# Optimization experiments

Measured on AMD Instinct MI355X. Metric: run time of the kernel, lower is better.

## Reference

```python
import jax, jax.numpy as jnp
import numpy as np

MAXV = 8  # convex quad clipped by 4 half-planes has <= 8 vertices


def decode(enc, anchors):
    """ResidualCoder.decode_torch for 7-dof lidar boxes (x,y,z,dx,dy,dz,r)."""
    xa, ya, za, dxa, dya, dza, ra = [anchors[..., i] for i in range(7)]
    xt, yt, zt, dxt, dyt, dzt, rt = [enc[..., i] for i in range(7)]
    diag = jnp.sqrt(dxa * dxa + dya * dya)
    xg = xt * diag + xa
    yg = yt * diag + ya
    zg = zt * dza + za
    dxg = jnp.exp(dxt) * dxa
    dyg = jnp.exp(dyt) * dya
    dzg = jnp.exp(dzt) * dza
    rg = rt + ra
    return jnp.stack([xg, yg, zg, dxg, dyg, dzg, rg], axis=-1)


def bev_corners(boxes):
    # boxes (...,7) -> CCW BEV corners (...,4,2) using x,y,dx,dy,heading
    x, y, dx, dy, r = boxes[..., 0], boxes[..., 1], boxes[..., 3], boxes[..., 4], boxes[..., 6]
    cx = jnp.stack([dx, -dx, -dx, dx], -1) * 0.5
    cy = jnp.stack([dy, dy, -dy, -dy], -1) * 0.5
    c, s = jnp.cos(r)[..., None], jnp.sin(r)[..., None]
    px = cx * c - cy * s + x[..., None]
    py = cx * s + cy * c + y[..., None]
    return jnp.stack([px, py], -1)


def _clip(poly, n, A, B):
    """Sutherland-Hodgman clip of polygon (poly[:n]) by half-plane left of A->B."""
    idx = jnp.arange(MAXV)
    e = B - A
    s = e[0] * (poly[:, 1] - A[1]) - e[1] * (poly[:, 0] - A[0])  # signed side
    prev = (idx - 1) % jnp.maximum(n, 1)
    s_prev = s[prev]
    p_prev = poly[prev]
    active = idx < n
    cin = s >= 0
    pin = s_prev >= 0
    den = s_prev - s
    t = s_prev / jnp.where(den == 0, 1.0, den)
    inter = p_prev + t[:, None] * (poly - p_prev)
    f_int = active & (cin != pin)   # edge crosses boundary -> emit intersection
    f_cur = active & cin            # current vertex inside -> emit it
    cand = jnp.stack([inter, poly], 1).reshape(2 * MAXV, 2)
    flags = jnp.stack([f_int, f_cur], 1).reshape(2 * MAXV)
    pos = jnp.cumsum(flags) - 1
    new_n = pos[-1] + 1
    pos = jnp.where(flags, pos, MAXV)  # invalid -> dump slot
    out = jnp.zeros((MAXV + 1, 2), poly.dtype).at[pos].set(cand)[:MAXV]
    return out, new_n.astype(jnp.int32)


def _pair_iou_bev(c1, c2, a1, a2):
    # c1,c2: (4,2) CCW corners of the two rotated BEV boxes; a1,a2: scalar areas
    poly = jnp.zeros((MAXV, 2), c1.dtype).at[:4].set(c1)
    n = jnp.asarray(4, jnp.int32)
    for e in range(4):
        poly, n = _clip(poly, n, c2[e], c2[(e + 1) % 4])
    idx = jnp.arange(MAXV)
    nxt = (idx + 1) % jnp.maximum(n, 1)
    x, y = poly[:, 0], poly[:, 1]
    contrib = jnp.where(idx < n, x * y[nxt] - x[nxt] * y, 0.0)
    inter = 0.5 * jnp.abs(contrib.sum())
    return inter / jnp.clip(a1 + a2 - inter, 1e-6, None)


def rotated_iou_bev_diag(boxes1, boxes2):
    """Diagonal (elementwise) rotated BEV IoU for flattened (M,7) lidar boxes."""
    c1 = bev_corners(boxes1)
    c2 = bev_corners(boxes2)
    a1 = boxes1[..., 3] * boxes1[..., 4]
    a2 = boxes2[..., 3] * boxes2[..., 4]
    return jax.vmap(_pair_iou_bev)(c1, c2, a1, a2)


def setup_inputs() -> dict:
    key = jax.random.key(0)
    ks = jax.random.split(key, 8)
    B, N = 4, 262144
    iou_preds = jax.random.normal(ks[0], (B, N), jnp.float32)
    one_hot_targets = jax.random.randint(ks[1], (B, N), 0, 2, jnp.int32)
    weights = jax.random.uniform(ks[2], (B, N), jnp.float32)
    # realistic anchors: xy in [-50,50], z ~ -1, dims in [1.5,4.5], heading in [0,pi)
    xy = jax.random.uniform(ks[3], (N, 2), jnp.float32, -50.0, 50.0)
    z = jnp.full((N, 1), -1.0, jnp.float32)
    dims = jax.random.uniform(ks[4], (N, 3), jnp.float32, 1.5, 4.5)
    ang = jax.random.uniform(ks[5], (N, 1), jnp.float32, 0.0, np.pi)
    anchors = jnp.concatenate([xy, z, dims, ang], axis=-1)
    box_preds = 0.1 * jax.random.normal(ks[6], (B, N, 7), jnp.float32)
    reg_targets = 0.1 * jax.random.normal(ks[7], (B, N, 7), jnp.float32)
    return {"iou_preds": iou_preds, "one_hot_targets": one_hot_targets,
            "weights": weights, "anchors": anchors,
            "box_preds": box_preds, "reg_targets": reg_targets}


def reference(iou_preds, one_hot_targets, weights, anchors, box_preds, reg_targets):
    B, N = iou_preds.shape
    dec_pred = decode(box_preds, anchors[None, :, :])   # (B,N,7)
    dec_tgt = decode(reg_targets, anchors[None, :, :])  # (B,N,7)
    iou = rotated_iou_bev_diag(dec_pred.reshape(B * N, 7),
                               dec_tgt.reshape(B * N, 7)).reshape(B, N)
    # label is computed with no grad, only at positive anchors; zero elsewhere
    target = jax.lax.stop_gradient(jnp.where(one_hot_targets > 0, iou, 0.0))
    # faithful to the original quirk: BCE-with-logits applied to sigmoid(iou_preds)
    z = jax.nn.sigmoid(iou_preds)
    p_t = jnp.logaddexp(0.0, z) - z * target  # log(1+e^z) - t*z
    return p_t * weights
```

## Files before the change

kernel.cpp:

```cpp
#include <hip/hip_runtime.h>
#include <math.h>

#define BLK 256


__device__ __forceinline__ float clamp_mag(float x) {
    return copysignf(fmaxf(fabsf(x), 1e-30f), x);
}

__device__ __forceinline__ void edge_piece(float px, float py, float ex, float ey,
                                           float rx, float ry, float hx, float hy,
                                           float& area2, float& Dx, float& Dy)
{
    float sx0 = (-hx - px) * rx, sx1 = (hx - px) * rx;
    float sy0 = (-hy - py) * ry, sy1 = (hy - py) * ry;
    float smin = fmaxf(fmaxf(fminf(sx0, sx1), fminf(sy0, sy1)), 0.0f);
    float smax = fminf(fminf(fmaxf(sx0, sx1), fmaxf(sy0, sy1)), 1.0f);
    smax = fmaxf(smax, smin);
    float ax = fmaf(smin, ex, px), ay = fmaf(smin, ey, py);
    float bx = fmaf(smax, ex, px), by = fmaf(smax, ey, py);
    float ux = bx - ax, uy = by - ay;
    area2 += fmaf(ax, uy, -(ay * ux));
    Dx += ux; Dy += uy;
}

__device__ __forceinline__ float pair_loss(const float bp[5], const float rt[5],
                                           float xa, float ya, float dxa, float dya,
                                           float ra, float diag,
                                           float ip, int oh, float w)
{
    float x1  = fmaf(bp[0], diag, xa);
    float y1  = fmaf(bp[1], diag, ya);
    float dx1 = __expf(bp[2]) * dxa;
    float dy1 = __expf(bp[3]) * dya;
    float r1  = bp[4] + ra;

    float x2  = fmaf(rt[0], diag, xa);
    float y2  = fmaf(rt[1], diag, ya);
    float dx2 = __expf(rt[2]) * dxa;
    float dy2 = __expf(rt[3]) * dya;
    float r2  = rt[4] + ra;

    float a1 = dx1 * dy1, a2 = dx2 * dy2;
    float h1x = 0.5f * dx1, h1y = 0.5f * dy1;
    float h2x = 0.5f * dx2, h2y = 0.5f * dy2;

    float c2v = __cosf(r2), s2v = __sinf(r2);
    float dr  = r1 - r2;
    float cd  = __cosf(dr), sd = __sinf(dr);
    float ddx = x1 - x2, ddy = y1 - y2;
    float tx  = fmaf(c2v, ddx,  s2v * ddy);
    float ty  = fmaf(-s2v, ddx, c2v * ddy);

    float ux_ = h1x * cd,  uy_ = h1x * sd;
    float vx_ = -h1y * sd, vy_ = h1y * cd;
    float eux = 2.0f * ux_, euy = 2.0f * uy_;
    float evx = 2.0f * vx_, evy = 2.0f * vy_;
    float ruxP = __fdividef(1.0f, clamp_mag(eux));
    float ruyP = __fdividef(1.0f, clamp_mag(euy));
    float rvxP = __fdividef(1.0f, clamp_mag(evx));
    float rvyP = __fdividef(1.0f, clamp_mag(evy));
    float p0x = tx + ux_ + vx_, p0y = ty + uy_ + vy_;
    float p1x = tx - ux_ + vx_, p1y = ty - uy_ + vy_;
    float p2x = tx - ux_ - vx_, p2y = ty - uy_ - vy_;
    float p3x = tx + ux_ - vx_, p3y = ty + uy_ - vy_;

    float area2 = 0.0f, dDx = 0.0f, dDy = 0.0f;
    edge_piece(p0x, p0y, -eux, -euy, -ruxP, -ruyP, h2x, h2y, area2, dDx, dDy);
    edge_piece(p1x, p1y, -evx, -evy, -rvxP, -rvyP, h2x, h2y, area2, dDx, dDy);
    edge_piece(p2x, p2y,  eux,  euy,  ruxP,  ruyP, h2x, h2y, area2, dDx, dDy);
    edge_piece(p3x, p3y,  evx,  evy,  rvxP,  rvyP, h2x, h2y, area2, dDx, dDy);

    float upx = h2x * cd,  upy = -h2x * sd;
    float vpx = h2y * sd,  vpy = h2y * cd;
    float ox  = -(fmaf(cd, tx,  sd * ty));
    float oy  = -(fmaf(-sd, tx, cd * ty));
    float equx = 2.0f * upx, equy = 2.0f * upy;
    float eqvx = 2.0f * vpx, eqvy = 2.0f * vpy;
    float ruxQ = __fdividef(1.0f, clamp_mag(equx));
    float ruyQ = __fdividef(1.0f, clamp_mag(equy));
    float rvxQ = __fdividef(1.0f, clamp_mag(eqvx));
    float rvyQ = __fdividef(1.0f, clamp_mag(eqvy));
    float q0x = ox + upx + vpx, q0y = oy + upy + vpy;
    float q1x = ox - upx + vpx, q1y = oy - upy + vpy;
    float q2x = ox - upx - vpx, q2y = oy - upy - vpy;
    float q3x = ox + upx - vpx, q3y = oy + upy - vpy;

    float Dx = 0.0f, Dy = 0.0f;
    edge_piece(q0x, q0y, -equx, -equy, -ruxQ, -ruyQ, h1x, h1y, area2, Dx, Dy);
    edge_piece(q1x, q1y, -eqvx, -eqvy, -rvxQ, -rvyQ, h1x, h1y, area2, Dx, Dy);
    edge_piece(q2x, q2y,  equx,  equy,  ruxQ,  ruyQ, h1x, h1y, area2, Dx, Dy);
    edge_piece(q3x, q3y,  eqvx,  eqvy,  rvxQ,  rvyQ, h1x, h1y, area2, Dx, Dy);

    float RDx = fmaf(cd, Dx, -(sd * Dy));
    float RDy = fmaf(sd, Dx,   cd * Dy);
    area2 += fmaf(tx, RDy, -(ty * RDx));

    float inter = 0.5f * fabsf(area2);
    float uni = fmaxf(a1 + a2 - inter, 1e-6f);
    float iou = __fdividef(inter, uni);

    float target = (oh > 0) ? iou : 0.0f;
    float z  = __fdividef(1.0f, 1.0f + __expf(-ip));
    float pt = __logf(1.0f + __expf(z)) - z * target;
    return pt * w;
}

__global__ __launch_bounds__(BLK)
void iou_pred_loss_kernel(const float* __restrict__ iou_preds,
                          const int*   __restrict__ one_hot,
                          const float* __restrict__ weights,
                          const float* __restrict__ anchors,
                          const float* __restrict__ box_preds,
                          const float* __restrict__ reg_targets,
                          float* __restrict__ out,
                          int N, int B)
{
    int tid   = threadIdx.x;
    int n_idx = blockIdx.x * BLK + tid;
    if (n_idx >= N) return;

    int yspan = gridDim.y;
    int b0 = blockIdx.y;
    int b1 = blockIdx.y + yspan;
    bool has2 = (b1 < B);
    size_t g0 = (size_t)b0 * N + n_idx;
    size_t g1 = (size_t)(has2 ? b1 : b0) * N + n_idx;

    const float* an = anchors + (size_t)n_idx * 7;
    float xa = an[0], ya = an[1], dxa = an[3], dya = an[4], ra = an[6];

    const float* bpp0 = box_preds   + g0 * 7;
    const float* rtp0 = reg_targets + g0 * 7;
    const float* bpp1 = box_preds   + g1 * 7;
    const float* rtp1 = reg_targets + g1 * 7;
    float bp0[5] = {bpp0[0], bpp0[1], bpp0[3], bpp0[4], bpp0[6]};
    float rt0[5] = {rtp0[0], rtp0[1], rtp0[3], rtp0[4], rtp0[6]};
    float bp1[5] = {bpp1[0], bpp1[1], bpp1[3], bpp1[4], bpp1[6]};
    float rt1[5] = {rtp1[0], rtp1[1], rtp1[3], rtp1[4], rtp1[6]};
    float ip0 = iou_preds[g0], ip1 = iou_preds[g1];
    int   oh0 = one_hot[g0],   oh1 = one_hot[g1];
    float w0  = weights[g0],   w1  = weights[g1];

    float diag = sqrtf(fmaf(dxa, dxa, dya * dya));

    out[g0] = pair_loss(bp0, rt0, xa, ya, dxa, dya, ra, diag, ip0, oh0, w0);
    if (has2)
        out[g1] = pair_loss(bp1, rt1, xa, ya, dxa, dya, ra, diag, ip1, oh1, w1);
}

extern "C" void kernel_launch(void* const* d_in, const int* in_sizes, int n_in,
                              void* d_out, int out_size, void* d_ws, size_t ws_size,
                              hipStream_t stream) {
    const float* iou_preds   = (const float*)d_in[0];
    const int*   one_hot     = (const int*)  d_in[1];
    const float* weights     = (const float*)d_in[2];
    const float* anchors     = (const float*)d_in[3];
    const float* box_preds   = (const float*)d_in[4];
    const float* reg_targets = (const float*)d_in[5];
    float* out = (float*)d_out;

    int total = in_sizes[0];
    int N     = in_sizes[3] / 7;
    int B     = total / N;

    dim3 grid((N + BLK - 1) / BLK, (B + 1) / 2);
    iou_pred_loss_kernel<<<grid, dim3(BLK), 0, stream>>>(
        iou_preds, one_hot, weights, anchors, box_preds, reg_targets,
        out, N, B);
}
```

Baseline: 111.6 us.

## Factor edge reciprocals into shared cos/sin/dim inverses and process four batches per thread

The eight per-edge reciprocals are replaced by six shared reciprocals (of cos, sin and the four box dimensions) whose products give the same inverse edge components. The batch loop is widened from two to four batch items per thread, with the grid y dimension shrunk to match, so the anchor load and diag are amortised further. This cuts division work and loads but raises register pressure, which may lower occupancy. Extra batch slots past B are now computed redundantly instead of skipped.

Measured after the change: 114.8 us. +2.9%, slower.

```diff
diff --git a/kernel.cpp b/kernel.cpp
--- a/kernel.cpp
+++ b/kernel.cpp
@@ -2,6 +2,7 @@
 #include <math.h>
 
 #define BLK 256
+#define UB  4
 
 
 __device__ __forceinline__ float clamp_mag(float x) {
@@ -52,14 +53,19 @@
     float tx  = fmaf(c2v, ddx,  s2v * ddy);
     float ty  = fmaf(-s2v, ddx, c2v * ddy);
 
+    float rcd  = __fdividef(1.0f, clamp_mag(cd));
+    float rsd  = __fdividef(1.0f, clamp_mag(sd));
+    float rdx1 = __fdividef(1.0f, dx1);
+    float rdy1 = __fdividef(1.0f, dy1);
+    float rdx2 = __fdividef(1.0f, dx2);
+    float rdy2 = __fdividef(1.0f, dy2);
+
     float ux_ = h1x * cd,  uy_ = h1x * sd;
     float vx_ = -h1y * sd, vy_ = h1y * cd;
-    float eux = 2.0f * ux_, euy = 2.0f * uy_;
-    float evx = 2.0f * vx_, evy = 2.0f * vy_;
-    float ruxP = __fdividef(1.0f, clamp_mag(eux));
-    float ruyP = __fdividef(1.0f, clamp_mag(euy));
-    float rvxP = __fdividef(1.0f, clamp_mag(evx));
-    float rvyP = __fdividef(1.0f, clamp_mag(evy));
+    float eux = dx1 * cd,  euy = dx1 * sd;
+    float evx = -dy1 * sd, evy = dy1 * cd;
+    float ruxP = rdx1 * rcd,    ruyP = rdx1 * rsd;
+    float rvxP = -(rdy1 * rsd), rvyP = rdy1 * rcd;
     float p0x = tx + ux_ + vx_, p0y = ty + uy_ + vy_;
     float p1x = tx - ux_ + vx_, p1y = ty - uy_ + vy_;
     float p2x = tx - ux_ - vx_, p2y = ty - uy_ - vy_;
@@ -75,12 +81,10 @@
     float vpx = h2y * sd,  vpy = h2y * cd;
     float ox  = -(fmaf(cd, tx,  sd * ty));
     float oy  = -(fmaf(-sd, tx, cd * ty));
-    float equx = 2.0f * upx, equy = 2.0f * upy;
-    float eqvx = 2.0f * vpx, eqvy = 2.0f * vpy;
-    float ruxQ = __fdividef(1.0f, clamp_mag(equx));
-    float ruyQ = __fdividef(1.0f, clamp_mag(equy));
-    float rvxQ = __fdividef(1.0f, clamp_mag(eqvx));
-    float rvyQ = __fdividef(1.0f, clamp_mag(eqvy));
+    float equx = dx2 * cd, equy = -dx2 * sd;
+    float eqvx = dy2 * sd, eqvy = dy2 * cd;
+    float ruxQ = rdx2 * rcd, ruyQ = -(rdx2 * rsd);
+    float rvxQ = rdy2 * rsd, rvyQ = rdy2 * rcd;
     float q0x = ox + upx + vpx, q0y = oy + upy + vpy;
     float q1x = ox - upx + vpx, q1y = oy - upy + vpy;
     float q2x = ox - upx - vpx, q2y = oy - upy - vpy;
@@ -121,32 +125,41 @@
     if (n_idx >= N) return;
 
     int yspan = gridDim.y;
-    int b0 = blockIdx.y;
-    int b1 = blockIdx.y + yspan;
-    bool has2 = (b1 < B);
-    size_t g0 = (size_t)b0 * N + n_idx;
-    size_t g1 = (size_t)(has2 ? b1 : b0) * N + n_idx;
+    size_t g[UB];
+    bool   has[UB];
+#pragma unroll
+    for (int k = 0; k < UB; ++k) {
+        int b  = blockIdx.y + k * yspan;
+        has[k] = (b < B);
+        g[k]   = (size_t)(has[k] ? b : 0) * N + n_idx;
+    }
 
     const float* an = anchors + (size_t)n_idx * 7;
     float xa = an[0], ya = an[1], dxa = an[3], dya = an[4], ra = an[6];
 
-    const float* bpp0 = box_preds   + g0 * 7;
-    const float* rtp0 = reg_targets + g0 * 7;
-    const float* bpp1 = box_preds   + g1 * 7;
-    const float* rtp1 = reg_targets + g1 * 7;
-    float bp0[5] = {bpp0[0], bpp0[1], bpp0[3], bpp0[4], bpp0[6]};
-    float rt0[5] = {rtp0[0], rtp0[1], rtp0[3], rtp0[4], rtp0[6]};
-    float bp1[5] = {bpp1[0], bpp1[1], bpp1[3], bpp1[4], bpp1[6]};
-    float rt1[5] = {rtp1[0], rtp1[1], rtp1[3], rtp1[4], rtp1[6]};
-    float ip0 = iou_preds[g0], ip1 = iou_preds[g1];
-    int   oh0 = one_hot[g0],   oh1 = one_hot[g1];
-    float w0  = weights[g0],   w1  = weights[g1];
+    float bp[UB][5], rt[UB][5], ip[UB], w[UB];
+    int   oh[UB];
+#pragma unroll
+    for (int k = 0; k < UB; ++k) {
+        const float* bpp = box_preds   + g[k] * 7;
+        const float* rtp = reg_targets + g[k] * 7;
+        bp[k][0] = bpp[0]; bp[k][1] = bpp[1]; bp[k][2] = bpp[3];
+        bp[k][3] = bpp[4]; bp[k][4] = bpp[6];
+        rt[k][0] = rtp[0]; rt[k][1] = rtp[1]; rt[k][2] = rtp[3];
+        rt[k][3] = rtp[4]; rt[k][4] = rtp[6];
+        ip[k] = iou_preds[g[k]];
+        oh[k] = one_hot[g[k]];
+        w[k]  = weights[g[k]];
+    }
 
     float diag = sqrtf(fmaf(dxa, dxa, dya * dya));
 
-    out[g0] = pair_loss(bp0, rt0, xa, ya, dxa, dya, ra, diag, ip0, oh0, w0);
-    if (has2)
-        out[g1] = pair_loss(bp1, rt1, xa, ya, dxa, dya, ra, diag, ip1, oh1, w1);
+#pragma unroll
+    for (int k = 0; k < UB; ++k) {
+        float res = pair_loss(bp[k], rt[k], xa, ya, dxa, dya, ra, diag,
+                              ip[k], oh[k], w[k]);
+        if (has[k]) out[g[k]] = res;
+    }
 }
 
 extern "C" void kernel_launch(void* const* d_in, const int* in_sizes, int n_in,
@@ -164,7 +177,7 @@
     int N     = in_sizes[3] / 7;
     int B     = total / N;
 
-    dim3 grid((N + BLK - 1) / BLK, (B + 1) / 2);
+    dim3 grid((N + BLK - 1) / BLK, (B + UB - 1) / UB);
     iou_pred_loss_kernel<<<grid, dim3(BLK), 0, stream>>>(
         iou_preds, one_hot, weights, anchors, box_preds, reg_targets,
         out, N, B);
```
